# Performance work log

Hardware: AMD Instinct MI355X
Metric: run time of the kernel (lower is better)

The kernel has to match this reference:

```python
import jax, jax.numpy as jnp
import numpy as np

N = 100000
E = 1600000
IN_DIM = 64
HID = 64
OUT = 64
NCLS = 40
EPS_BN = 1e-5


def _sym_norms(src, dst, n):
    # DGL GraphConv norm='both': src scaled by out_degree^-1/2, dst by in_degree^-1/2,
    # degrees clamped to min 1.
    ones = jnp.ones(src.shape[0], dtype=jnp.float32)
    deg_out = jax.ops.segment_sum(ones, src, num_segments=n)
    deg_in = jax.ops.segment_sum(ones, dst, num_segments=n)
    return jnp.clip(deg_out, 1.0) ** -0.5, jnp.clip(deg_in, 1.0) ** -0.5


def _graph_conv(x, src, dst, norm_src, norm_dst, W, b):
    # D_dst^{-1/2} A D_src^{-1/2} X W + b
    x = x * norm_src[:, None]
    agg = jax.ops.segment_sum(x[src], dst, num_segments=x.shape[0])
    agg = agg * norm_dst[:, None]
    return agg @ W + b


def _gcn(x, src, dst, W1, b1, W2, b2):
    ns, nd = _sym_norms(src, dst, x.shape[0])
    h = jax.nn.relu(_graph_conv(x, src, dst, ns, nd, W1, b1))
    return _graph_conv(h, src, dst, ns, nd, W2, b2)


def setup_inputs() -> dict:
    key = jax.random.key(0)
    ks = jax.random.split(key, 16)
    glorot = lambda k, fi, fo: jax.random.normal(k, (fi, fo), jnp.float32) * np.sqrt(2.0 / (fi + fo))
    return {
        "feat1": jax.random.normal(ks[0], (N, IN_DIM), jnp.float32),
        "src1": jax.random.randint(ks[1], (E,), 0, N, jnp.int32),
        "dst1": jax.random.randint(ks[2], (E,), 0, N, jnp.int32),
        "feat2": jax.random.normal(ks[3], (N, IN_DIM), jnp.float32),
        "src2": jax.random.randint(ks[4], (E,), 0, N, jnp.int32),
        "dst2": jax.random.randint(ks[5], (E,), 0, N, jnp.int32),
        "W1a": glorot(ks[6], IN_DIM, HID), "b1a": jnp.zeros(HID, jnp.float32),
        "W1b": glorot(ks[7], HID, OUT), "b1b": jnp.zeros(OUT, jnp.float32),
        "W2a": glorot(ks[8], IN_DIM, HID), "b2a": jnp.zeros(HID, jnp.float32),
        "W2b": glorot(ks[9], HID, OUT), "b2b": jnp.zeros(OUT, jnp.float32),
        "Wm1": glorot(ks[10], OUT, HID), "bm1": jnp.zeros(HID, jnp.float32),
        "gamma": jnp.ones(HID, jnp.float32), "beta": jnp.zeros(HID, jnp.float32),
        "Wm2": glorot(ks[11], HID, NCLS), "bm2": jnp.zeros(NCLS, jnp.float32),
    }


def reference(feat1, src1, dst1, feat2, src2, dst2,
              W1a, b1a, W1b, b1b, W2a, b2a, W2b, b2b,
              Wm1, bm1, gamma, beta, Wm2, bm2):
    h1 = _gcn(feat1, src1, dst1, W1a, b1a, W1b, b1b)
    h2 = _gcn(feat2, src2, dst2, W2a, b2a, W2b, b2b)
    # torch .std() is unbiased (ddof=1)
    z1 = (h1 - h1.mean(0)) / jnp.std(h1, axis=0, ddof=1)
    z2 = (h2 - h2.mean(0)) / jnp.std(h2, axis=0, ddof=1)
    z = (z1 + z2) * 0.5
    # MLP2 head: Linear -> BatchNorm1d (training-mode batch stats) -> ReLU -> Linear
    y = z @ Wm1 + bm1
    mu = y.mean(0)
    var = y.var(0)  # biased, as BN uses
    y = (y - mu) * jax.lax.rsqrt(var + EPS_BN) * gamma + beta
    pred_y = jax.nn.relu(y) @ Wm2 + bm2
    return (z1, z2, pred_y)
```

## Files before the change

kernel.cpp:

```cpp
#include <hip/hip_runtime.h>
#include <hip/hip_bf16.h>

#define DIM 64
#define NCLS_OUT 40
#define BSH 8
#define BROWS 256
#define BIN_CHUNK 12288

typedef __hip_bfloat16 bf16;

__device__ __forceinline__ float lane_bcast(float v, int l) {
  return __int_as_float(__builtin_amdgcn_readlane(__float_as_int(v), l));
}
__device__ __forceinline__ unsigned short f2bf_bits(float f) {
  bf16 h = __float2bfloat16(f);
  return *reinterpret_cast<unsigned short*>(&h);
}

__device__ __forceinline__ float ldf(const void* p, long i, int m) {
  return m ? ((const float*)p)[i] : __bfloat162float(((const bf16*)p)[i]);
}
__device__ __forceinline__ void stf(void* p, long i, float v, int m) {
  if (m) ((float*)p)[i] = v;
  else ((bf16*)p)[i] = __float2bfloat16(v);
}

__global__ void k_detect(const unsigned int* __restrict__ wds, int nw, int* __restrict__ mode) {
  __shared__ int cnt_s;
  if (threadIdx.x == 0) cnt_s = 0;
  __syncthreads();
  int c = 0;
  for (int i = threadIdx.x; i < nw; i += 1024) {
    unsigned h = wds[i] & 0xFFFFu;
    unsigned e = (h >> 7) & 0xFFu;
    if (e == 0xFFu || (e != 0u && e < 0x60u)) c++;
  }
  atomicAdd(&cnt_s, c);
  __syncthreads();
  if (threadIdx.x == 0) *mode = (cnt_s > nw / 16) ? 1 : 0;
}

__global__ void k_deg_out(const int* __restrict__ src1, const int* __restrict__ src2,
                          int* __restrict__ deg, int n, int e1, int etot) {
  int i = blockIdx.x * 256 + threadIdx.x;
  if (i >= etot) return;
  if (i < e1) atomicAdd(&deg[2 * n + src1[i]], 1);
  else atomicAdd(&deg[3 * n + src2[i - e1]], 1);
}

__global__ void k_norm(const int* __restrict__ deg, float* __restrict__ nrm, int n4) {
  int i = blockIdx.x * 256 + threadIdx.x;
  if (i < n4) {
    int d = deg[i];
    if (d < 1) d = 1;
    nrm[i] = rsqrtf((float)d);
  }
}

__global__ void k_bhist(const int* __restrict__ dst1, const int* __restrict__ dst2,
                        int* __restrict__ bh, int n, int e1, int etot, int NB) {
  extern __shared__ int cnt[];
  for (int b = threadIdx.x; b < NB; b += blockDim.x) cnt[b] = 0;
  __syncthreads();
  int stride = gridDim.x * blockDim.x;
  for (int i = blockIdx.x * blockDim.x + threadIdx.x; i < etot; i += stride) {
    int row = (i < e1) ? dst1[i] : (n + dst2[i - e1]);
    atomicAdd(&cnt[row >> BSH], 1);
  }
  __syncthreads();
  for (int b = threadIdx.x; b < NB; b += blockDim.x)
    if (cnt[b]) atomicAdd(&bh[b], cnt[b]);
}

__global__ void k_bscan(const int* __restrict__ bh, int* __restrict__ bbase,
                        int* __restrict__ gcur, int* __restrict__ rp,
                        int NB, int etot, int n2) {
  __shared__ int sm[256];
  __shared__ int carry_s;
  int t = threadIdx.x;
  if (t == 0) carry_s = 0;
  __syncthreads();
  for (int base = 0; base < NB; base += 256) {
    int i = base + t;
    int v = (i < NB) ? bh[i] : 0;
    sm[t] = v;
    __syncthreads();
    for (int o = 1; o < 256; o <<= 1) {
      int a = (t >= o) ? sm[t - o] : 0;
      __syncthreads();
      sm[t] += a;
      __syncthreads();
    }
    int c = carry_s;
    int excl = c + sm[t] - v;
    int tot = sm[255];
    __syncthreads();
    if (i < NB) { bbase[i] = excl; gcur[i] = excl; }
    if (t == 0) carry_s = c + tot;
    __syncthreads();
  }
  if (t == 0) { bbase[NB] = etot; rp[n2] = etot; }
}

__global__ void __launch_bounds__(256) k_bin(
    const int* __restrict__ src1, const int* __restrict__ dst1,
    const int* __restrict__ src2, const int* __restrict__ dst2,
    int* __restrict__ gcur, unsigned* __restrict__ eb,
    int n, int e1, int etot, int NB) {
  extern __shared__ int lds[];
  int* cnt = lds;
  int* base = lds + NB;
  int t = threadIdx.x;
  int c0 = blockIdx.x * BIN_CHUNK;
  int cend = c0 + BIN_CHUNK;
  if (cend > etot) cend = etot;
  for (int b = t; b < NB; b += 256) cnt[b] = 0;
  __syncthreads();
  for (int i = c0 + t; i < cend; i += 256) {
    int row = (i < e1) ? dst1[i] : (n + dst2[i - e1]);
    atomicAdd(&cnt[row >> BSH], 1);
  }
  __syncthreads();
  for (int b = t; b < NB; b += 256) {
    int c = cnt[b];
    base[b] = c ? atomicAdd(&gcur[b], c) : 0;
    cnt[b] = 0;
  }
  __syncthreads();
  for (int i = c0 + t; i < cend; i += 256) {
    int s, row;
    if (i < e1) { s = src1[i]; row = dst1[i]; }
    else { s = src2[i - e1]; row = n + dst2[i - e1]; }
    int b = row >> BSH;
    int l = atomicAdd(&cnt[b], 1);
    eb[base[b] + l] = ((unsigned)(row & (BROWS - 1)) << 24) | (unsigned)s;
  }
}

__global__ void __launch_bounds__(256) k_fine(
    const unsigned* __restrict__ eb, const int* __restrict__ bbase,
    int* __restrict__ rp, int* __restrict__ deg, int* __restrict__ sb,
    int n2, int NB) {
  __shared__ int hist[256];
  __shared__ int sm[256];
  __shared__ int curs[256];
  int t = threadIdx.x;
  for (int b = blockIdx.x; b < NB; b += gridDim.x) {
    int ebeg = bbase[b], eend = bbase[b + 1];
    hist[t] = 0;
    __syncthreads();
    for (int i = ebeg + t; i < eend; i += 256)
      atomicAdd(&hist[eb[i] >> 24], 1);
    __syncthreads();
    int v = hist[t];
    sm[t] = v;
    __syncthreads();
    for (int o = 1; o < 256; o <<= 1) {
      int a = (t >= o) ? sm[t - o] : 0;
      __syncthreads();
      sm[t] += a;
      __syncthreads();
    }
    int excl = sm[t] - v;
    int row = (b << BSH) + t;
    if (row < n2) { deg[row] = v; rp[row] = ebeg + excl; }
    curs[t] = excl;
    __syncthreads();
    for (int i = ebeg + t; i < eend; i += 256) {
      unsigned u = eb[i];
      int l = atomicAdd(&curs[u >> 24], 1);
      sb[ebeg + l] = (int)(u & 0xFFFFFFu);
    }
    __syncthreads();
  }
}

__global__ void k_scale_all(const void* __restrict__ f1, const void* __restrict__ f2,
                            const float* __restrict__ norms, bf16* __restrict__ P,
                            int n, const int* __restrict__ mode) {
  int m = *mode;
  int i = blockIdx.x * 256 + threadIdx.x;
  int nd = n * DIM;
  if (i >= 2 * nd) return;
  int g = i >= nd;
  int li = g ? i - nd : i;
  float ns = norms[2 * n + g * n + (li >> 6)];
  P[i] = __float2bfloat16(ldf(g ? f2 : f1, li, m) * ns);
}

__global__ void k_scale_one(const void* __restrict__ f, const float* __restrict__ ns,
                            bf16* __restrict__ P, int nd, const int* __restrict__ mode) {
  int m = *mode;
  int i = blockIdx.x * 256 + threadIdx.x;
  if (i < nd) P[i] = __float2bfloat16(ldf(f, i, m) * ns[i >> 6]);
}

__global__ void __launch_bounds__(256) k_gmm(
    const bf16* __restrict__ X, const int* __restrict__ rp, const int* __restrict__ sb,
    const void* __restrict__ Wg0, const void* __restrict__ bg0,
    const void* __restrict__ Wg1, const void* __restrict__ bg1,
    const float* __restrict__ pre0, const float* __restrict__ pre1,
    const float* __restrict__ post0, const float* __restrict__ post1,
    bf16* __restrict__ Y, int n, int relu, const int* __restrict__ mode,
    int dual, int gsel, float* __restrict__ stats) {
  __shared__ __align__(16) char xs[4][8192];
  int m = *mode;
  int t = threadIdx.x, lane = t & 63, wid = t >> 6;
  int g = dual ? (blockIdx.x & 1) : gsel;
  int ord = dual ? (blockIdx.x >> 1) : blockIdx.x;
  int nblk = dual ? (gridDim.x >> 1) : gridDim.x;
  int rowbase = dual ? g * n : 0;
  const char* Xb = (const char*)X + ((long)rowbase << 7);
  char* xsw = xs[wid];

  const void* W = g ? Wg1 : Wg0;
  const void* bb = g ? bg1 : bg0;
  const float* pre = g ? pre1 : pre0;
  const float* post = g ? post1 : post0;

  unsigned wp[32];
#pragma unroll
  for (int i = 0; i < 32; ++i) {
    unsigned lb = f2bf_bits(ldf(W, (2 * i) * 64 + lane, m));
    unsigned hb = f2bf_bits(ldf(W, (2 * i + 1) * 64 + lane, m));
    wp[i] = lb | (hb << 16);
  }
  float bias = ldf(bb, lane, m);
  float ps = 0.f, pq = 0.f;

  int swz = lane & 7;
  int stride = nblk * 4;
  const int* rpg = rp + (long)g * n;
  int node = ord * 4 + wid;
  int b0 = 0, e0 = 0;
  if (node < n) { b0 = rpg[node]; e0 = rpg[node + 1]; }
  for (; node < n; node += stride) {
    int nn = node + stride;
    int nb0 = 0, ne0 = 0;
    if (nn < n) { nb0 = rpg[nn]; ne0 = rpg[nn + 1]; }
    float a0 = 0.f, a1 = 0.f, a2 = 0.f, a3 = 0.f;
    for (int base = b0; base < e0; base += 64) {
      int cnt = e0 - base;
      if (cnt > 64) cnt = 64;
      int li = (lane < cnt) ? lane : 0;
      int eidx = sb[base + li];
      const uint4* rowp = (const uint4*)(Xb + ((long)eidx << 7));
      uint4 r0 = rowp[0], r1 = rowp[1], r2 = rowp[2], r3 = rowp[3];
      uint4 r4 = rowp[4], r5 = rowp[5], r6 = rowp[6], r7 = rowp[7];
      uint4* wrow = (uint4*)(xsw + lane * 128);
      wrow[0 ^ swz] = r0; wrow[1 ^ swz] = r1;
      wrow[2 ^ swz] = r2; wrow[3 ^ swz] = r3;
      wrow[4 ^ swz] = r4; wrow[5 ^ swz] = r5;
      wrow[6 ^ swz] = r6; wrow[7 ^ swz] = r7;
#define RD(J, K) __uint_as_float((unsigned)(*(const unsigned short*)(             \
        xsw + ((J) + (K)) * 128 + ((lane << 1) ^ ((K) << 4)))) << 16)
      int j = 0;
      for (; j + 8 <= cnt; j += 8) {
        a0 += RD(j, 0); a1 += RD(j, 1); a2 += RD(j, 2); a3 += RD(j, 3);
        a0 += RD(j, 4); a1 += RD(j, 5); a2 += RD(j, 6); a3 += RD(j, 7);
      }
      for (; j < cnt; ++j) {
        a0 += __uint_as_float((unsigned)(*(const unsigned short*)(
            xsw + j * 128 + ((lane << 1) ^ ((j & 7) << 4)))) << 16);
      }
#undef RD
    }
    float acc = (a0 + a1) + (a2 + a3);
    acc *= pre[node];
    float r = 0.f;
#pragma unroll
    for (int i = 0; i < 32; ++i) {
      r = fmaf(lane_bcast(acc, 2 * i), __uint_as_float(wp[i] << 16), r);
      r = fmaf(lane_bcast(acc, 2 * i + 1), __uint_as_float(wp[i] & 0xFFFF0000u), r);
    }
    r += bias;
    if (relu) r = fmaxf(r, 0.f);
    if (post) r *= post[node];
    Y[(long)(rowbase + node) * DIM + lane] = __float2bfloat16(r);
    ps += r;
    pq += r * r;
    b0 = nb0; e0 = ne0;
  }

  if (stats) {
    __syncthreads();
    float* ssum = (float*)xs;
    float* ssq = ssum + 256;
    ssum[wid * 64 + lane] = ps;
    ssq[wid * 64 + lane] = pq;
    __syncthreads();
    if (t < 64) {
      float a = ssum[t] + ssum[64 + t] + ssum[128 + t] + ssum[192 + t];
      float b2 = ssq[t] + ssq[64 + t] + ssq[128 + t] + ssq[192 + t];
      atomicAdd(&stats[g * 128 + t], a);
      atomicAdd(&stats[g * 128 + 64 + t], b2);
    }
  }
}

__global__ void __launch_bounds__(256) k_mm64s(const bf16* __restrict__ X,
                                               const void* __restrict__ W,
                                               const void* __restrict__ b,
                                               bf16* __restrict__ Y, int n,
                                               const int* __restrict__ mode,
                                               float* __restrict__ stats) {
  int m = *mode;
  int t = threadIdx.x, lane = t & 63, wid = t >> 6;
  float w[64];
#pragma unroll
  for (int k = 0; k < 64; ++k) w[k] = ldf(W, k * 64 + lane, m);
  float bias = ldf(b, lane, m);
  float ps = 0.f, pq = 0.f;
  int stride = gridDim.x * 4;
  for (int row = blockIdx.x * 4 + wid; row < n; row += stride) {
    float a = __bfloat162float(X[(long)row * 64 + lane]);
    float acc = 0.f;
#pragma unroll
    for (int k = 0; k < 64; ++k) acc = fmaf(lane_bcast(a, k), w[k], acc);
    acc += bias;
    Y[(long)row * 64 + lane] = __float2bfloat16(acc);
    ps += acc;
    pq += acc * acc;
  }
  __shared__ float ssum[4][64], ssq[4][64];
  ssum[wid][lane] = ps;
  ssq[wid][lane] = pq;
  __syncthreads();
  if (t < 64) {
    float a = ssum[0][t] + ssum[1][t] + ssum[2][t] + ssum[3][t];
    float b2 = ssq[0][t] + ssq[1][t] + ssq[2][t] + ssq[3][t];
    atomicAdd(&stats[t], a);
    atomicAdd(&stats[64 + t], b2);
  }
}

__global__ void k_z_dual(const bf16* __restrict__ H, const float* __restrict__ stats,
                         void* __restrict__ zout, bf16* __restrict__ Dz, int n,
                         const int* __restrict__ mode) {
  int m = *mode;
  int i = blockIdx.x * 256 + threadIdx.x;
  int nd = n * DIM;
  if (i >= nd) return;
  int c = i & 63;
  float fn = (float)n;
  float mu1 = stats[c] / fn;
  float var1 = fmaxf((stats[64 + c] - mu1 * mu1 * fn) / (fn - 1.0f), 1e-12f);
  float mu2 = stats[128 + c] / fn;
  float var2 = fmaxf((stats[192 + c] - mu2 * mu2 * fn) / (fn - 1.0f), 1e-12f);
  float z1 = (__bfloat162float(H[i]) - mu1) * rsqrtf(var1);
  float z2 = (__bfloat162float(H[nd + i]) - mu2) * rsqrtf(var2);
  stf(zout, i, z1, m);
  stf(zout, (long)nd + i, z2, m);
  Dz[i] = __float2bfloat16(0.5f * (z1 + z2));
}

__global__ void k_z_seq(const bf16* __restrict__ h, const float* __restrict__ stats,
                        void* __restrict__ zout, long zoff, bf16* __restrict__ zacc,
                        int n, int init, const int* __restrict__ mode) {
  int m = *mode;
  int i = blockIdx.x * 256 + threadIdx.x;
  if (i >= n * DIM) return;
  int c = i & 63;
  float fn = (float)n;
  float mu = stats[c] / fn;
  float var = fmaxf((stats[64 + c] - mu * mu * fn) / (fn - 1.0f), 1e-12f);
  float z = (__bfloat162float(h[i]) - mu) * rsqrtf(var);
  stf(zout, zoff + i, z, m);
  float prev = init ? 0.f : __bfloat162float(zacc[i]);
  zacc[i] = __float2bfloat16(prev + 0.5f * z);
}

__global__ void __launch_bounds__(256) k_head(const bf16* __restrict__ Yv,
                                              const float* __restrict__ s,
                                              const float* __restrict__ sq,
                                              const void* __restrict__ gamma,
                                              const void* __restrict__ beta,
                                              const void* __restrict__ W2,
                                              const void* __restrict__ b2,
                                              void* __restrict__ out, long ooff, int n,
                                              const int* __restrict__ mode) {
  int m = *mode;
  int t = threadIdx.x, lane = t & 63, wid = t >> 6;
  float w[64];
#pragma unroll
  for (int k = 0; k < 64; ++k)
    w[k] = (lane < NCLS_OUT) ? ldf(W2, k * NCLS_OUT + lane, m) : 0.f;
  float bias = (lane < NCLS_OUT) ? ldf(b2, lane, m) : 0.f;
  float fn = (float)n;
  float mu = s[lane] / fn;
  float var = sq[lane] / fn - mu * mu;
  float rstd = rsqrtf(fmaxf(var, 0.f) + 1e-5f);
  float g = ldf(gamma, lane, m);
  float be = ldf(beta, lane, m);
  int stride = gridDim.x * 4;
  for (int row = blockIdx.x * 4 + wid; row < n; row += stride) {
    float yv = __bfloat162float(Yv[(long)row * 64 + lane]);
    float yn = fmaxf((yv - mu) * rstd * g + be, 0.f);
    float acc = bias;
#pragma unroll
    for (int k = 0; k < 64; ++k) acc = fmaf(lane_bcast(yn, k), w[k], acc);
    if (lane < NCLS_OUT) stf(out, ooff + (long)row * NCLS_OUT + lane, acc, m);
  }
}

extern "C" void kernel_launch(void* const* d_in, const int* in_sizes, int n_in,
                              void* d_out, int out_size, void* d_ws, size_t ws_size,
                              hipStream_t stream) {
  const void* feat1 = d_in[0];
  const int* src1 = (const int*)d_in[1];
  const int* dst1 = (const int*)d_in[2];
  const void* feat2 = d_in[3];
  const int* src2 = (const int*)d_in[4];
  const int* dst2 = (const int*)d_in[5];
  const void* W1a = d_in[6];
  const void* b1a = d_in[7];
  const void* W1b = d_in[8];
  const void* b1b = d_in[9];
  const void* W2a = d_in[10];
  const void* b2a = d_in[11];
  const void* W2b = d_in[12];
  const void* b2b = d_in[13];
  const void* Wm1 = d_in[14];
  const void* bm1 = d_in[15];
  const void* gamma = d_in[16];
  const void* beta = d_in[17];
  const void* Wm2 = d_in[18];
  const void* bm2 = d_in[19];

  const int n = in_sizes[0] / DIM;
  const int e1 = in_sizes[1];
  const int e2 = in_sizes[4];
  const int etot = e1 + e2;
  const long nd = (long)n * DIM;
  const int NB = (2 * n + BROWS - 1) >> BSH;

  char* w = (char*)d_ws;
  size_t off = 0;
  auto alloc = [&](size_t bytes) -> void* {
    void* p = w + off;
    off += (bytes + 255) & ~(size_t)255;
    return p;
  };
  int* mode = (int*)alloc(256);
  int* deg = (int*)alloc((size_t)4 * n * 4);
  float* stats = (float*)alloc(512 * 4);
  float* norms = (float*)alloc((size_t)4 * n * 4);
  int* rp = (int*)alloc((size_t)(2 * n + 8) * 4);
  int* bh = (int*)alloc((size_t)(NB + 1) * 4);
  int* bbase = (int*)alloc((size_t)(NB + 1) * 4);
  int* gcur = (int*)alloc((size_t)(NB + 1) * 4);
  int* sb = (int*)alloc((size_t)etot * 4);
  size_t base_off = off;
  bool dual = (ws_size >= base_off + (size_t)5 * nd * 2 + 4096);

  bf16 *P, *Q, *Dz;
  size_t qbytes;
  if (dual) {
    P = (bf16*)alloc((size_t)2 * nd * 2);
    Q = (bf16*)alloc((size_t)2 * nd * 2);
    Dz = (bf16*)alloc((size_t)nd * 2);
    qbytes = (size_t)2 * nd * 2;
  } else {
    P = (bf16*)alloc((size_t)nd * 2);
    Q = (bf16*)alloc((size_t)nd * 2);
    Dz = (bf16*)alloc((size_t)nd * 2);
    qbytes = (size_t)nd * 2;
  }
  unsigned* eb = ((size_t)etot * 4 <= qbytes) ? (unsigned*)Q
                                              : (unsigned*)alloc((size_t)etot * 4);

  const float* nd1 = norms;
  const float* nd2 = norms + n;
  const float* ns1 = norms + 2 * n;
  const float* ns2 = norms + 3 * n;

  int gE = (etot + 255) / 256;
  int gND = (int)((nd + 255) / 256);
  int g2ND = (int)((2 * nd + 255) / 256);
  int g4N = (4 * n + 255) / 256;
  int gBIN = (etot + BIN_CHUNK - 1) / BIN_CHUNK;
  const int gGMM = 4096;

  hipMemsetAsync(deg + 2 * n, 0, (size_t)2 * n * 4, stream);
  hipMemsetAsync(stats, 0, 512 * 4, stream);
  hipMemsetAsync(bh, 0, (size_t)NB * 4, stream);

  k_detect<<<1, 1024, 0, stream>>>((const unsigned int*)feat1, 8192, mode);
  k_deg_out<<<gE, 256, 0, stream>>>(src1, src2, deg, n, e1, etot);

  k_bhist<<<256, 256, (size_t)NB * 4, stream>>>(dst1, dst2, bh, n, e1, etot, NB);
  k_bscan<<<1, 256, 0, stream>>>(bh, bbase, gcur, rp, NB, etot, 2 * n);
  k_bin<<<gBIN, 256, (size_t)2 * NB * 4, stream>>>(src1, dst1, src2, dst2, gcur, eb,
                                                   n, e1, etot, NB);
  k_fine<<<NB, 256, 0, stream>>>(eb, bbase, rp, deg, sb, 2 * n, NB);
  k_norm<<<g4N, 256, 0, stream>>>(deg, norms, 4 * n);

  if (dual) {
    k_scale_all<<<g2ND, 256, 0, stream>>>(feat1, feat2, norms, P, n, mode);
    k_gmm<<<gGMM, 256, 0, stream>>>(P, rp, sb, W1a, b1a, W2a, b2a, nd1, nd2, ns1, ns2,
                                    Q, n, 1, mode, 1, 0, (float*)nullptr);
    k_gmm<<<gGMM, 256, 0, stream>>>(Q, rp, sb, W1b, b1b, W2b, b2b, nd1, nd2,
                                    (const float*)nullptr, (const float*)nullptr,
                                    P, n, 0, mode, 1, 0, stats);
    k_z_dual<<<gND, 256, 0, stream>>>(P, stats, d_out, Dz, n, mode);
  } else {
    k_scale_one<<<gND, 256, 0, stream>>>(feat1, ns1, P, (int)nd, mode);
    k_gmm<<<gGMM, 256, 0, stream>>>(P, rp, sb, W1a, b1a, W1a, b1a, nd1, nd1, ns1, ns1,
                                    Q, n, 1, mode, 0, 0, (float*)nullptr);
    k_gmm<<<gGMM, 256, 0, stream>>>(Q, rp, sb, W1b, b1b, W1b, b1b, nd1, nd1,
                                    (const float*)nullptr, (const float*)nullptr,
                                    P, n, 0, mode, 0, 0, stats);
    k_z_seq<<<gND, 256, 0, stream>>>(P, stats, d_out, 0L, Dz, n, 1, mode);
    k_scale_one<<<gND, 256, 0, stream>>>(feat2, ns2, P, (int)nd, mode);
    k_gmm<<<gGMM, 256, 0, stream>>>(P, rp, sb, W2a, b2a, W2a, b2a, nd2, nd2, ns2, ns2,
                                    Q, n, 1, mode, 0, 1, (float*)nullptr);
    k_gmm<<<gGMM, 256, 0, stream>>>(Q, rp, sb, W2b, b2b, W2b, b2b, nd2, nd2,
                                    (const float*)nullptr, (const float*)nullptr,
                                    P, n, 0, mode, 0, 1, stats + 128);
    k_z_seq<<<gND, 256, 0, stream>>>(P, stats + 128, d_out, nd, Dz, n, 0, mode);
  }

  k_mm64s<<<512, 256, 0, stream>>>(Dz, Wm1, bm1, Q, n, mode, stats + 256);
  k_head<<<512, 256, 0, stream>>>(Q, stats + 256, stats + 320, gamma, beta, Wm2, bm2,
                                  d_out, 2 * nd, n, mode);
}
```

Baseline: 1.075 ms.

## Gather neighbor rows directly per lane with double-buffered loads instead of LDS staging

Replaces the LDS-staged gather in the fused aggregate+matmul kernel. Previously each lane loaded a whole 128-byte neighbor row into shared memory and then read it back transposed. Now every lane reads its own 2-byte feature column from each neighbor row, broadcasting indices with readlane and double-buffering 8-row batches to keep loads in flight. This drops the 32KB LDS buffer, which should raise occupancy, but it issues many small 2-byte global loads per lane in place of wide 16-byte loads.

```diff
diff --git a/kernel.cpp b/kernel.cpp
--- a/kernel.cpp
+++ b/kernel.cpp
@@ -203,7 +203,6 @@
     const float* __restrict__ post0, const float* __restrict__ post1,
     bf16* __restrict__ Y, int n, int relu, const int* __restrict__ mode,
     int dual, int gsel, float* __restrict__ stats) {
-  __shared__ __align__(16) char xs[4][8192];
   int m = *mode;
   int t = threadIdx.x, lane = t & 63, wid = t >> 6;
   int g = dual ? (blockIdx.x & 1) : gsel;
@@ -211,7 +210,6 @@
   int nblk = dual ? (gridDim.x >> 1) : gridDim.x;
   int rowbase = dual ? g * n : 0;
   const char* Xb = (const char*)X + ((long)rowbase << 7);
-  char* xsw = xs[wid];
 
   const void* W = g ? Wg1 : Wg0;
   const void* bb = g ? bg1 : bg0;
@@ -228,7 +226,6 @@
   float bias = ldf(bb, lane, m);
   float ps = 0.f, pq = 0.f;
 
-  int swz = lane & 7;
   int stride = nblk * 4;
   const int* rpg = rp + (long)g * n;
   int node = ord * 4 + wid;
@@ -242,28 +239,44 @@
     for (int base = b0; base < e0; base += 64) {
       int cnt = e0 - base;
       if (cnt > 64) cnt = 64;
-      int li = (lane < cnt) ? lane : 0;
-      int eidx = sb[base + li];
-      const uint4* rowp = (const uint4*)(Xb + ((long)eidx << 7));
-      uint4 r0 = rowp[0], r1 = rowp[1], r2 = rowp[2], r3 = rowp[3];
-      uint4 r4 = rowp[4], r5 = rowp[5], r6 = rowp[6], r7 = rowp[7];
-      uint4* wrow = (uint4*)(xsw + lane * 128);
-      wrow[0 ^ swz] = r0; wrow[1 ^ swz] = r1;
-      wrow[2 ^ swz] = r2; wrow[3 ^ swz] = r3;
-      wrow[4 ^ swz] = r4; wrow[5 ^ swz] = r5;
-      wrow[6 ^ swz] = r6; wrow[7 ^ swz] = r7;
-#define RD(J, K) __uint_as_float((unsigned)(*(const unsigned short*)(             \
-        xsw + ((J) + (K)) * 128 + ((lane << 1) ^ ((K) << 4)))) << 16)
-      int j = 0;
-      for (; j + 8 <= cnt; j += 8) {
-        a0 += RD(j, 0); a1 += RD(j, 1); a2 += RD(j, 2); a3 += RD(j, 3);
-        a0 += RD(j, 4); a1 += RD(j, 5); a2 += RD(j, 6); a3 += RD(j, 7);
+      int cm = cnt - 1;
+      int eidx = (lane < cnt) ? sb[base + lane] : 0;
+      unsigned short A[8], B[8];
+
+#define GISS(V, J)                                                              \
+      { _Pragma("unroll") for (int k = 0; k < 8; ++k) {                         \
+          int ii = (J) + k; if (ii > cm) ii = cm;                               \
+          int s = __builtin_amdgcn_readlane(eidx, ii);                          \
+          V[k] = *(const unsigned short*)(Xb + ((long)(unsigned)s << 7)         \
+                                          + (lane << 1));                       \
+        } }
+#define GCON(V, J)                                                              \
+      { int rem = cnt - (J);                                                    \
+        if (rem >= 8) {                                                         \
+          _Pragma("unroll") for (int k = 0; k < 8; ++k) {                       \
+            float f = __uint_as_float((unsigned)V[k] << 16);                    \
+            if ((k & 3) == 0) a0 += f; else if ((k & 3) == 1) a1 += f;          \
+            else if ((k & 3) == 2) a2 += f; else a3 += f;                       \
+          }                                                                     \
+        } else {                                                                \
+          _Pragma("unroll") for (int k = 0; k < 8; ++k) if (k < rem) {          \
+            float f = __uint_as_float((unsigned)V[k] << 16);                    \
+            if ((k & 3) == 0) a0 += f; else if ((k & 3) == 1) a1 += f;          \
+            else if ((k & 3) == 2) a2 += f; else a3 += f;                       \
+          }                                                                     \
+        } }
+
+      GISS(A, 0);
+      for (int j = 0;; j += 16) {
+        if (j + 8 < cnt) GISS(B, j + 8);
+        GCON(A, j);
+        if (j + 8 >= cnt) break;
+        if (j + 16 < cnt) GISS(A, j + 16);
+        GCON(B, j + 8);
+        if (j + 16 >= cnt) break;
       }
-      for (; j < cnt; ++j) {
-        a0 += __uint_as_float((unsigned)(*(const unsigned short*)(
-            xsw + j * 128 + ((lane << 1) ^ ((j & 7) << 4)))) << 16);
-      }
-#undef RD
+#undef GISS
+#undef GCON
     }
     float acc = (a0 + a1) + (a2 + a3);
     acc *= pre[node];
@@ -283,15 +296,13 @@
   }
 
   if (stats) {
-    __syncthreads();
-    float* ssum = (float*)xs;
-    float* ssq = ssum + 256;
-    ssum[wid * 64 + lane] = ps;
-    ssq[wid * 64 + lane] = pq;
+    __shared__ float ssum[4][64], ssq[4][64];
+    ssum[wid][lane] = ps;
+    ssq[wid][lane] = pq;
     __syncthreads();
     if (t < 64) {
-      float a = ssum[t] + ssum[64 + t] + ssum[128 + t] + ssum[192 + t];
-      float b2 = ssq[t] + ssq[64 + t] + ssq[128 + t] + ssq[192 + t];
+      float a = ssum[0][t] + ssum[1][t] + ssum[2][t] + ssum[3][t];
+      float b2 = ssq[0][t] + ssq[1][t] + ssq[2][t] + ssq[3][t];
       atomicAdd(&stats[g * 128 + t], a);
       atomicAdd(&stats[g * 128 + 64 + t], b2);
     }
```

New measurement: 1.002 ms. 6.8% less time.
